# Performance work log

Measured on AMD Instinct MI355X. Metric: run time of the kernel, lower is better.

The kernel has to match this reference:

```python
import jax, jax.numpy as jnp
import numpy as np

NA = 40000   # author nodes
NP = 40000   # paper nodes
E = 800000   # edges per relation
HID = 64
HOP = 5
SEM = 128


def setup_inputs() -> dict:
    key = jax.random.key(0)
    ks = jax.random.split(key, 32)
    f32 = jnp.float32
    rn = lambda k, s, sc=0.1: jax.random.normal(k, s, f32) * sc
    inp = {}
    inp["x_author"] = jax.random.normal(ks[0], (NA, 334), f32)
    inp["x_paper"] = jax.random.normal(ks[1], (NP, 512), f32)
    inp["W1_a"] = rn(ks[2], (334, HID), 0.05)
    inp["b1_a"] = jnp.zeros((HID,), f32)
    inp["W1_p"] = rn(ks[3], (512, HID), 0.05)
    inp["b1_p"] = jnp.zeros((HID,), f32)
    inp["a1_ap"] = rn(ks[4], (HOP, HID))
    inp["a2_ap"] = rn(ks[5], (HOP, HID))
    inp["a1_aa"] = rn(ks[6], (HOP, HID))
    inp["a2_aa"] = rn(ks[7], (HOP, HID))
    inp["a1_pa"] = rn(ks[8], (HOP, HID))
    inp["a2_pa"] = rn(ks[9], (HOP, HID))
    inp["a1_pp"] = rn(ks[10], (HOP, HID))
    inp["a2_pp"] = rn(ks[11], (HOP, HID))
    inp["semW_a"] = rn(ks[12], (HOP, HID, SEM))
    inp["semb_a"] = jnp.zeros((HOP, SEM), f32)
    inp["semq_a"] = rn(ks[13], (HOP, SEM))
    inp["semW_p"] = rn(ks[14], (HOP, HID, SEM))
    inp["semb_p"] = jnp.zeros((HOP, SEM), f32)
    inp["semq_p"] = rn(ks[15], (HOP, SEM))
    inp["W2"] = rn(ks[16], (HID, 4))
    inp["b2"] = jnp.zeros((4,), f32)
    inp["ei_ap"] = jax.random.randint(ks[17], (2, E), 0, NA)  # row0=src(author) row1=tgt(paper)
    inp["ei_aa"] = jax.random.randint(ks[18], (2, E), 0, NA)
    inp["ei_pa"] = jax.random.randint(ks[19], (2, E), 0, NP)
    inp["ei_pp"] = jax.random.randint(ks[20], (2, E), 0, NP)
    return inp


def _leaky(v):
    return jnp.where(v > 0.0, v, 0.2 * v)


def _edge_agg(x, h, s, t, a1, a2, n):
    # x: [Ns,D] source features (fixed), h: [Nt,D] current target state
    x1 = x @ a1                                   # [Ns]
    h1 = h @ a2                                   # [Nt]
    w2 = jnp.exp(_leaky(x1 + x @ a2))             # [Ns] self-loop score
    w1 = jnp.exp(_leaky(x1[s] + h1[t]))           # [E]  edge score
    div = jax.ops.segment_sum(w1, s, num_segments=n) + w2
    num = jax.ops.segment_sum(w1[:, None] * h[t], s, num_segments=n) + w2[:, None] * x
    return num / div[:, None]


def _sem(z, W, b, q):
    # z: [N,M,D]; HAN-style semantic attention over M relations
    sc = jnp.tanh(jnp.einsum('nmd,dk->nmk', z, W) + b) @ q   # [N,M]
    beta = jax.nn.softmax(jnp.mean(sc, axis=0))               # [M]
    return jnp.einsum('m,nmd->nd', beta, z)


def reference(x_author, x_paper, W1_a, b1_a, W1_p, b1_p,
              a1_ap, a2_ap, a1_aa, a2_aa, a1_pa, a2_pa, a1_pp, a2_pp,
              semW_a, semb_a, semq_a, semW_p, semb_p, semq_p,
              W2, b2, ei_ap, ei_aa, ei_pa, ei_pp):
    # eval mode: dropout is identity
    xA = jax.nn.relu(x_author @ W1_a + b1_a)
    xP = jax.nn.relu(x_paper @ W1_p + b1_p)
    hA, hP = xA, xP
    nA, nP = xA.shape[0], xP.shape[0]
    for i in range(HOP):
        eA = jnp.stack([
            _edge_agg(xA, hP, ei_ap[0], ei_ap[1], a1_ap[i], a2_ap[i], nA),
            _edge_agg(xA, hA, ei_aa[0], ei_aa[1], a1_aa[i], a2_aa[i], nA)], axis=1)
        eP = jnp.stack([
            _edge_agg(xP, hA, ei_pa[0], ei_pa[1], a1_pa[i], a2_pa[i], nP),
            _edge_agg(xP, hP, ei_pp[0], ei_pp[1], a1_pp[i], a2_pp[i], nP)], axis=1)
        hA = jax.nn.elu(_sem(eA, semW_a[i], semb_a[i], semq_a[i]))
        hP = jax.nn.elu(_sem(eP, semW_p[i], semb_p[i], semq_p[i]))
    return hA @ W2 + b2   # target_node_type = 'author'
```

## Files before the change

kernel.cpp:

```cpp
#include <hip/hip_runtime.h>
#include <hip/hip_fp16.h>

#define NN 40000
#define DD 64
#define EE 800000
#define NHOP 5
#define NSEM 128
#define NBK 625
#define BINCH 8192

__device__ __forceinline__ float leaky02(float v) { return v > 0.f ? v : 0.2f * v; }
__device__ __forceinline__ float tanh_fast(float x) {
  return 1.f - 2.f / (__expf(2.f * x) + 1.f);
}
__device__ __forceinline__ float wred(float x) {
  #pragma unroll
  for (int m = 1; m < 64; m <<= 1) x += __shfl_xor(x, m);
  return x;
}

__global__ void zero_i32(int* __restrict__ p, int n) {
  int i = blockIdx.x * blockDim.x + threadIdx.x;
  if (i < n) p[i] = 0;
}

#define PBM 64
#define PBK 32
__global__ __launch_bounds__(256) void proj_gemm_relu2(
    const float* __restrict__ Xa, const float* __restrict__ Wa,
    const float* __restrict__ ba, float* __restrict__ oa, __half* __restrict__ oa16,
    const float* __restrict__ Xp, const float* __restrict__ Wp,
    const float* __restrict__ bp, float* __restrict__ op, __half* __restrict__ op16)
{
  int side = blockIdx.y;
  const float* X = side ? Xp : Xa;
  const float* W = side ? Wp : Wa;
  const float* bias = side ? bp : ba;
  float* out = side ? op : oa;
  __half* out16 = side ? op16 : oa16;
  int K = side ? 512 : 334;

  __shared__ float As[PBM][PBK + 1];
  __shared__ float Bs[PBK][DD];
  int tid = threadIdx.x;
  int tx = tid & 15;
  int ty = tid >> 4;
  int row0 = blockIdx.x * PBM;
  float acc[4][4] = {{0.f}};
  int nk = (K + PBK - 1) / PBK;
  for (int kt = 0; kt < nk; ++kt) {
    int k0 = kt * PBK;
    #pragma unroll
    for (int j = 0; j < 8; ++j) {
      int idx = tid + j * 256;
      int r = idx >> 5, c = idx & 31;
      int gk = k0 + c;
      As[r][c] = (gk < K) ? X[(size_t)(row0 + r) * K + gk] : 0.f;
    }
    #pragma unroll
    for (int j = 0; j < 2; ++j) {
      int idx = tid + j * 256;
      int r = idx >> 4, c4 = idx & 15;
      int gk = k0 + r;
      float4 v = (gk < K) ? ((const float4*)(W + (size_t)gk * DD))[c4]
                          : make_float4(0.f, 0.f, 0.f, 0.f);
      ((float4*)&Bs[r][0])[c4] = v;
    }
    __syncthreads();
    #pragma unroll 8
    for (int kk = 0; kk < PBK; ++kk) {
      float a0 = As[ty * 4 + 0][kk];
      float a1 = As[ty * 4 + 1][kk];
      float a2 = As[ty * 4 + 2][kk];
      float a3 = As[ty * 4 + 3][kk];
      float4 bv = ((float4*)&Bs[kk][0])[tx];
      acc[0][0] = fmaf(a0, bv.x, acc[0][0]);
      acc[0][1] = fmaf(a0, bv.y, acc[0][1]);
      acc[0][2] = fmaf(a0, bv.z, acc[0][2]);
      acc[0][3] = fmaf(a0, bv.w, acc[0][3]);
      acc[1][0] = fmaf(a1, bv.x, acc[1][0]);
      acc[1][1] = fmaf(a1, bv.y, acc[1][1]);
      acc[1][2] = fmaf(a1, bv.z, acc[1][2]);
      acc[1][3] = fmaf(a1, bv.w, acc[1][3]);
      acc[2][0] = fmaf(a2, bv.x, acc[2][0]);
      acc[2][1] = fmaf(a2, bv.y, acc[2][1]);
      acc[2][2] = fmaf(a2, bv.z, acc[2][2]);
      acc[2][3] = fmaf(a2, bv.w, acc[2][3]);
      acc[3][0] = fmaf(a3, bv.x, acc[3][0]);
      acc[3][1] = fmaf(a3, bv.y, acc[3][1]);
      acc[3][2] = fmaf(a3, bv.z, acc[3][2]);
      acc[3][3] = fmaf(a3, bv.w, acc[3][3]);
    }
    __syncthreads();
  }
  float4 bb = ((const float4*)bias)[tx];
  #pragma unroll
  for (int i = 0; i < 4; ++i) {
    int gr = row0 + ty * 4 + i;
    float4 v;
    v.x = fmaxf(acc[i][0] + bb.x, 0.f);
    v.y = fmaxf(acc[i][1] + bb.y, 0.f);
    v.z = fmaxf(acc[i][2] + bb.z, 0.f);
    v.w = fmaxf(acc[i][3] + bb.w, 0.f);
    ((float4*)(out + (size_t)gr * DD))[tx] = v;
    __half2 p0 = __floats2half2_rn(v.x, v.y);
    __half2 p1 = __floats2half2_rn(v.z, v.w);
    ((__half2*)(out16 + (size_t)gr * DD))[tx * 2 + 0] = p0;
    ((__half2*)(out16 + (size_t)gr * DD))[tx * 2 + 1] = p1;
  }
}

__global__ __launch_bounds__(256) void binCount_kernel(
    const int* __restrict__ e0, const int* __restrict__ e1,
    const int* __restrict__ e2, const int* __restrict__ e3,
    int* __restrict__ bcnt, int e)
{
  int rel = blockIdx.y;
  const int* S = rel == 0 ? e0 : rel == 1 ? e1 : rel == 2 ? e2 : e3;
  __shared__ int cnt[NBK];
  int tid = threadIdx.x;
  for (int b = tid; b < NBK; b += 256) cnt[b] = 0;
  __syncthreads();
  int e0i = blockIdx.x * BINCH;
  int ne = min(BINCH, e - e0i);
  for (int i = tid; i < ne; i += 256) atomicAdd(&cnt[S[e0i + i] >> 6], 1);
  __syncthreads();
  for (int b = tid; b < NBK; b += 256)
    if (cnt[b]) atomicAdd(&bcnt[rel * NBK + b], cnt[b]);
}

__global__ __launch_bounds__(1024) void bucketScan_kernel(
    const int* __restrict__ bcnt, int* __restrict__ bbase, int* __restrict__ bcur,
    int* __restrict__ rp0, int* __restrict__ rp1, int* __restrict__ rp2,
    int* __restrict__ rp3, int e)
{
  int rel = blockIdx.x;
  __shared__ int sh[1024];
  int t = threadIdx.x;
  int v = (t < NBK) ? bcnt[rel * NBK + t] : 0;
  sh[t] = v;
  __syncthreads();
  for (int off = 1; off < 1024; off <<= 1) {
    int y = (t >= off) ? sh[t - off] : 0;
    __syncthreads();
    sh[t] += y;
    __syncthreads();
  }
  if (t < NBK) {
    int base = sh[t] - v;
    bbase[rel * (NBK + 1) + t] = base;
    bcur[rel * NBK + t] = base;
  }
  if (t == 0) {
    bbase[rel * (NBK + 1) + NBK] = e;
    (rel == 0 ? rp0 : rel == 1 ? rp1 : rel == 2 ? rp2 : rp3)[NN] = e;
  }
}

__global__ __launch_bounds__(256) void binA_kernel(
    const int* __restrict__ e0, const int* __restrict__ e1,
    const int* __restrict__ e2, const int* __restrict__ e3,
    int* __restrict__ bcur, unsigned* __restrict__ pairbuf, int e)
{
  int rel = blockIdx.y;
  const int* S = rel == 0 ? e0 : rel == 1 ? e1 : rel == 2 ? e2 : e3;
  const int* T = S + e;
  unsigned* pb = pairbuf + (size_t)rel * e;
  __shared__ int cnt[NBK], base[NBK], cnt2[NBK];
  int tid = threadIdx.x;
  for (int b = tid; b < NBK; b += 256) { cnt[b] = 0; cnt2[b] = 0; }
  __syncthreads();
  int e0i = blockIdx.x * BINCH;
  int ne = min(BINCH, e - e0i);
  for (int i = tid; i < ne; i += 256) atomicAdd(&cnt[S[e0i + i] >> 6], 1);
  __syncthreads();
  for (int b = tid; b < NBK; b += 256)
    base[b] = cnt[b] ? atomicAdd(&bcur[rel * NBK + b], cnt[b]) : 0;
  __syncthreads();
  for (int i = tid; i < ne; i += 256) {
    int s = S[e0i + i];
    int t = T[e0i + i];
    int b = s >> 6;
    int off = atomicAdd(&cnt2[b], 1);
    pb[base[b] + off] = ((unsigned)(s & 63) << 16) | (unsigned)t;
  }
}

__global__ __launch_bounds__(256) void binB_kernel(
    const unsigned* __restrict__ pairbuf, const int* __restrict__ bbase,
    int* __restrict__ rp0, int* __restrict__ rp1, int* __restrict__ rp2,
    int* __restrict__ rp3,
    unsigned short* __restrict__ ts0, unsigned short* __restrict__ ts1,
    unsigned short* __restrict__ ts2, unsigned short* __restrict__ ts3, int e)
{
  int rel = blockIdx.y;
  int* rowptr = rel == 0 ? rp0 : rel == 1 ? rp1 : rel == 2 ? rp2 : rp3;
  unsigned short* ts = rel == 0 ? ts0 : rel == 1 ? ts1 : rel == 2 ? ts2 : ts3;
  const unsigned* pb = pairbuf + (size_t)rel * e;
  int b = blockIdx.x;
  int bstart = bbase[rel * (NBK + 1) + b];
  int bend   = bbase[rel * (NBK + 1) + b + 1];
  __shared__ int ncnt[64], cur[64];
  int tid = threadIdx.x;
  if (tid < 64) ncnt[tid] = 0;
  __syncthreads();
  for (int i = bstart + tid; i < bend; i += 256)
    atomicAdd(&ncnt[(pb[i] >> 16) & 63], 1);
  __syncthreads();
  if (tid < 64) {
    int v = ncnt[tid];
    int x = v;
    #pragma unroll
    for (int off = 1; off < 64; off <<= 1) {
      int y = __shfl_up(x, off);
      if (tid >= off) x += y;
    }
    int nb = bstart + x - v;
    rowptr[b * 64 + tid] = nb;
    cur[tid] = nb;
  }
  __syncthreads();
  for (int i = bstart + tid; i < bend; i += 256) {
    unsigned u = pb[i];
    int pos = atomicAdd(&cur[(u >> 16) & 63], 1);
    ts[pos] = (unsigned short)(u & 0xffffu);
  }
}

__global__ __launch_bounds__(256) void precompute_xw(
    const float* __restrict__ xA, const float* __restrict__ xP,
    const float* __restrict__ a1_ap, const float* __restrict__ a2_ap,
    const float* __restrict__ a1_aa, const float* __restrict__ a2_aa,
    const float* __restrict__ a1_pa, const float* __restrict__ a2_pa,
    const float* __restrict__ a1_pp, const float* __restrict__ a2_pp,
    float* __restrict__ x1all, float* __restrict__ w2all,
    float* __restrict__ h1_ap, float* __restrict__ h1_aa,
    float* __restrict__ h1_pa, float* __restrict__ h1_pp)
{
  int side = blockIdx.y;
  __shared__ float L[21 * DD];
  int tid = threadIdx.x;
  {
    const float* s0 = side ? a1_pa : a1_ap;
    const float* s1 = side ? a2_pa : a2_ap;
    const float* s2 = side ? a1_pp : a1_aa;
    const float* s3 = side ? a2_pp : a2_aa;
    const float* ex = side ? a2_ap : a2_pa;
    for (int i = tid; i < 21 * DD; i += 256) {
      int k = i >> 6, d = i & 63;
      const float* src = (k < 5) ? s0 : (k < 10) ? s1 : (k < 15) ? s2 : (k < 20) ? s3 : ex;
      int hop = (k < 20) ? (k % 5) : 0;
      L[i] = src[hop * DD + d];
    }
  }
  __syncthreads();
  int j = blockIdx.x * 256 + tid;
  if (j >= NN) return;
  const float4* x4 = (const float4*)((side ? xP : xA) + (size_t)j * DD);
  float acc[21];
  #pragma unroll
  for (int k = 0; k < 21; ++k) acc[k] = 0.f;
  #pragma unroll
  for (int d0 = 0; d0 < 16; ++d0) {
    float4 v = x4[d0];
    #pragma unroll
    for (int c = 0; c < 4; ++c) {
      int d = d0 * 4 + c;
      float xv = (&v.x)[c];
      #pragma unroll
      for (int k = 0; k < 21; ++k) acc[k] = fmaf(xv, L[k * DD + d], acc[k]);
    }
  }
  int relA = side ? 2 : 0;
  #pragma unroll
  for (int i = 0; i < NHOP; ++i) {
    x1all[((size_t)(relA + 0) * NHOP + i) * NN + j] = acc[0 * 5 + i];
    w2all[((size_t)(relA + 0) * NHOP + i) * NN + j] =
        __expf(leaky02(acc[0 * 5 + i] + acc[1 * 5 + i]));
    x1all[((size_t)(relA + 1) * NHOP + i) * NN + j] = acc[2 * 5 + i];
    w2all[((size_t)(relA + 1) * NHOP + i) * NN + j] =
        __expf(leaky02(acc[2 * 5 + i] + acc[3 * 5 + i]));
  }
  if (side) { h1_pp[j] = acc[15]; h1_ap[j] = acc[20]; }
  else      { h1_aa[j] = acc[15]; h1_pa[j] = acc[20]; }
}

struct AggRel {
  const float* x; const __half2* h2; const float* x1; const float* w2; const float* h1;
  const int* rowptr; const unsigned short* tsorted; float* out;
};

__global__ __launch_bounds__(256) void agg4_kernel(AggRel r0, AggRel r1, AggRel r2,
                                                   AggRel r3, int n)
{
  int bid = blockIdx.x;
  int g = (bid >> 2) & 1;
  int u = (bid >> 3) * 4 + (bid & 3);
  int half = n >> 2;
  int relsel = u >= half;
  int nodeblk = relsel ? (u - half) : u;
  AggRel R;
  if (g == 0) R = relsel ? r2 : r1;
  else        R = relsel ? r3 : r0;

  int wid = nodeblk * 4 + (threadIdx.x >> 6);
  int lane = threadIdx.x & 63;
  int pair = lane >> 5;
  int c2 = lane & 31;

  int beg = R.rowptr[wid], end = R.rowptr[wid + 1];
  float x1i = R.x1[wid];
  float2 a0v = make_float2(0.f, 0.f), a1v = make_float2(0.f, 0.f);
  float2 a2v = make_float2(0.f, 0.f), a3v = make_float2(0.f, 0.f);
  float2 a4v = make_float2(0.f, 0.f), a5v = make_float2(0.f, 0.f);
  float2 a6v = make_float2(0.f, 0.f), a7v = make_float2(0.f, 0.f);
  float wsumL = 0.f;
  for (int c = beg; c < end; c += 64) {
    int idx = c + lane;
    int t = 0;
    float wv = 0.f;
    if (idx < end) {
      t = R.tsorted[idx];
      wv = __expf(leaky02(x1i + R.h1[t]));
    }
    wsumL += wv;
    int ne = min(64, end - c);
    for (int j = 0; j < ne; j += 16) {
      int s0 = j + pair,      s1 = j + 2 + pair,  s2 = j + 4 + pair,  s3 = j + 6 + pair;
      int s4 = j + 8 + pair,  s5 = j + 10 + pair, s6 = j + 12 + pair, s7 = j + 14 + pair;
      int t0 = __shfl(t, s0), t1 = __shfl(t, s1), t2 = __shfl(t, s2), t3 = __shfl(t, s3);
      int t4 = __shfl(t, s4), t5 = __shfl(t, s5), t6 = __shfl(t, s6), t7 = __shfl(t, s7);
      float w0 = __shfl(wv, s0), w1 = __shfl(wv, s1), w2_ = __shfl(wv, s2), w3 = __shfl(wv, s3);
      float w4 = __shfl(wv, s4), w5 = __shfl(wv, s5), w6 = __shfl(wv, s6), w7 = __shfl(wv, s7);
      float2 f0 = __half22float2(R.h2[((unsigned)t0 << 5) + c2]);
      float2 f1 = __half22float2(R.h2[((unsigned)t1 << 5) + c2]);
      float2 f2 = __half22float2(R.h2[((unsigned)t2 << 5) + c2]);
      float2 f3 = __half22float2(R.h2[((unsigned)t3 << 5) + c2]);
      float2 f4 = __half22float2(R.h2[((unsigned)t4 << 5) + c2]);
      float2 f5 = __half22float2(R.h2[((unsigned)t5 << 5) + c2]);
      float2 f6 = __half22float2(R.h2[((unsigned)t6 << 5) + c2]);
      float2 f7 = __half22float2(R.h2[((unsigned)t7 << 5) + c2]);
      a0v.x = fmaf(w0, f0.x, a0v.x);  a0v.y = fmaf(w0, f0.y, a0v.y);
      a1v.x = fmaf(w1, f1.x, a1v.x);  a1v.y = fmaf(w1, f1.y, a1v.y);
      a2v.x = fmaf(w2_, f2.x, a2v.x); a2v.y = fmaf(w2_, f2.y, a2v.y);
      a3v.x = fmaf(w3, f3.x, a3v.x);  a3v.y = fmaf(w3, f3.y, a3v.y);
      a4v.x = fmaf(w4, f4.x, a4v.x);  a4v.y = fmaf(w4, f4.y, a4v.y);
      a5v.x = fmaf(w5, f5.x, a5v.x);  a5v.y = fmaf(w5, f5.y, a5v.y);
      a6v.x = fmaf(w6, f6.x, a6v.x);  a6v.y = fmaf(w6, f6.y, a6v.y);
      a7v.x = fmaf(w7, f7.x, a7v.x);  a7v.y = fmaf(w7, f7.y, a7v.y);
    }
  }
  float wsum = wred(wsumL);
  float2 acc;
  acc.x = ((a0v.x + a1v.x) + (a2v.x + a3v.x)) + ((a4v.x + a5v.x) + (a6v.x + a7v.x));
  acc.y = ((a0v.y + a1v.y) + (a2v.y + a3v.y)) + ((a4v.y + a5v.y) + (a6v.y + a7v.y));
  acc.x += __shfl_xor(acc.x, 32);
  acc.y += __shfl_xor(acc.y, 32);
  if (pair == 0) {
    float w2v = R.w2[wid];
    float inv = 1.f / (wsum + w2v);
    float2 xv = ((const float2*)(R.x + (size_t)wid * DD))[c2];
    float2 o;
    o.x = fmaf(w2v, xv.x, acc.x) * inv;
    o.y = fmaf(w2v, xv.y, acc.y) * inv;
    ((float2*)(R.out + (size_t)wid * DD))[c2] = o;
  }
}

__global__ __launch_bounds__(256) void sem_kernel(
    const float* __restrict__ eA0, const float* __restrict__ eA1,
    const float* __restrict__ eP0, const float* __restrict__ eP1,
    const float* __restrict__ Wa, const float* __restrict__ ba, const float* __restrict__ qa,
    const float* __restrict__ Wp, const float* __restrict__ bp, const float* __restrict__ qp,
    float* __restrict__ psums)
{
  int side = blockIdx.y;
  const float* e0 = side ? eP0 : eA0;
  const float* e1 = side ? eP1 : eA1;
  const float* W = side ? Wp : Wa;
  const float* b = side ? bp : ba;
  const float* q = side ? qp : qa;

  __shared__ float Ws[DD * NSEM];
  __shared__ float zt[2][DD][12];
  __shared__ float red0[256], red1[256];
  int tid = threadIdx.x;
  {
    const float4* W4 = (const float4*)W;
    float4* Ws4 = (float4*)Ws;
    #pragma unroll
    for (int j = 0; j < 8; ++j) Ws4[tid + j * 256] = W4[tid + j * 256];
  }
  int slot = tid >> 7;
  int k = tid & 127;
  float bk = b[k], qk = q[k];
  int base = blockIdx.x * 64;
  float sum0 = 0.f, sum1 = 0.f;
  for (int it = 0; it < 8; ++it) {
    #pragma unroll
    for (int j = 0; j < 4; ++j) {
      int idx = tid + j * 256;
      int d = idx & 63, m = (idx >> 6) & 1, nn = idx >> 7;
      zt[m][d][nn] = (m ? e1 : e0)[(size_t)(base + it * 8 + nn) * DD + d];
    }
    __syncthreads();
    float a0[4], a1[4];
    #pragma unroll
    for (int nn = 0; nn < 4; ++nn) { a0[nn] = bk; a1[nn] = bk; }
    #pragma unroll 8
    for (int d = 0; d < DD; ++d) {
      float w = Ws[d * NSEM + k];
      float4 za = *(const float4*)&zt[0][d][slot * 4];
      float4 zb = *(const float4*)&zt[1][d][slot * 4];
      a0[0] = fmaf(za.x, w, a0[0]);
      a0[1] = fmaf(za.y, w, a0[1]);
      a0[2] = fmaf(za.z, w, a0[2]);
      a0[3] = fmaf(za.w, w, a0[3]);
      a1[0] = fmaf(zb.x, w, a1[0]);
      a1[1] = fmaf(zb.y, w, a1[1]);
      a1[2] = fmaf(zb.z, w, a1[2]);
      a1[3] = fmaf(zb.w, w, a1[3]);
    }
    #pragma unroll
    for (int nn = 0; nn < 4; ++nn) {
      sum0 += tanh_fast(a0[nn]) * qk;
      sum1 += tanh_fast(a1[nn]) * qk;
    }
    __syncthreads();
  }
  red0[tid] = sum0;
  red1[tid] = sum1;
  __syncthreads();
  for (int off = 128; off; off >>= 1) {
    if (tid < off) { red0[tid] += red0[tid + off]; red1[tid] += red1[tid + off]; }
    __syncthreads();
  }
  if (tid == 0) {
    int idx = (side * gridDim.x + blockIdx.x) * 2;
    psums[idx + 0] = red0[0];
    psums[idx + 1] = red1[0];
  }
}

__global__ __launch_bounds__(256) void beta_kernel(const float* __restrict__ psums,
    float* __restrict__ beta, int nblk, float invn)
{
  __shared__ float s[4][256];
  int t = threadIdx.x;
  float a0 = 0.f, a1 = 0.f, p0 = 0.f, p1 = 0.f;
  for (int i = t; i < nblk; i += 256) {
    a0 += psums[i * 2];
    a1 += psums[i * 2 + 1];
    p0 += psums[(nblk + i) * 2];
    p1 += psums[(nblk + i) * 2 + 1];
  }
  s[0][t] = a0; s[1][t] = a1; s[2][t] = p0; s[3][t] = p1;
  __syncthreads();
  for (int off = 128; off; off >>= 1) {
    if (t < off) {
      s[0][t] += s[0][t + off]; s[1][t] += s[1][t + off];
      s[2][t] += s[2][t + off]; s[3][t] += s[3][t + off];
    }
    __syncthreads();
  }
  if (t == 0) {
    float m0 = s[0][0] * invn, m1 = s[1][0] * invn;
    float mx = fmaxf(m0, m1);
    float x0 = __expf(m0 - mx), x1 = __expf(m1 - mx);
    float inv = 1.f / (x0 + x1);
    beta[0] = x0 * inv; beta[1] = x1 * inv;
    m0 = s[2][0] * invn; m1 = s[3][0] * invn;
    mx = fmaxf(m0, m1);
    x0 = __expf(m0 - mx); x1 = __expf(m1 - mx);
    inv = 1.f / (x0 + x1);
    beta[2] = x0 * inv; beta[3] = x1 * inv;
  }
}

__global__ void combine2_kernel(const float4* __restrict__ eA0, const float4* __restrict__ eA1,
    const float4* __restrict__ eP0, const float4* __restrict__ eP1,
    const float* __restrict__ beta, float4* __restrict__ hA, float4* __restrict__ hP,
    __half2* __restrict__ hA16, __half2* __restrict__ hP16,
    const float* __restrict__ a2_ap_n, const float* __restrict__ a2_aa_n,
    const float* __restrict__ a2_pa_n, const float* __restrict__ a2_pp_n,
    float* __restrict__ h1_ap, float* __restrict__ h1_aa,
    float* __restrict__ h1_pa, float* __restrict__ h1_pp,
    int has_next, int nvec)
{
  int side = blockIdx.y;
  int i = blockIdx.x * 256 + threadIdx.x;
  if (i >= nvec) return;
  float b0 = beta[side * 2], b1 = beta[side * 2 + 1];
  float4 v0 = (side ? eP0 : eA0)[i];
  float4 v1 = (side ? eP1 : eA1)[i];
  float4 r;
  float t;
  t = b0 * v0.x + b1 * v1.x; r.x = t > 0.f ? t : (__expf(t) - 1.f);
  t = b0 * v0.y + b1 * v1.y; r.y = t > 0.f ? t : (__expf(t) - 1.f);
  t = b0 * v0.z + b1 * v1.z; r.z = t > 0.f ? t : (__expf(t) - 1.f);
  t = b0 * v0.w + b1 * v1.w; r.w = t > 0.f ? t : (__expf(t) - 1.f);
  (side ? hP : hA)[i] = r;
  (side ? hP16 : hA16)[i * 2 + 0] = __floats2half2_rn(r.x, r.y);
  (side ? hP16 : hA16)[i * 2 + 1] = __floats2half2_rn(r.z, r.w);
  if (has_next) {
    int col4 = i & 15;
    const float* ax = side ? a2_ap_n : a2_aa_n;
    const float* ay = side ? a2_pp_n : a2_pa_n;
    float4 a4 = ((const float4*)ax)[col4];
    float4 c4 = ((const float4*)ay)[col4];
    float rx = r.x * a4.x + r.y * a4.y + r.z * a4.z + r.w * a4.w;
    float ry = r.x * c4.x + r.y * c4.y + r.z * c4.z + r.w * c4.w;
    #pragma unroll
    for (int m = 1; m < 16; m <<= 1) {
      rx += __shfl_xor(rx, m);
      ry += __shfl_xor(ry, m);
    }
    if ((threadIdx.x & 15) == 0) {
      int row = i >> 4;
      if (side) { h1_ap[row] = rx; h1_pp[row] = ry; }
      else      { h1_aa[row] = rx; h1_pa[row] = ry; }
    }
  }
}

__global__ void final_kernel(const float* __restrict__ hA, const float* __restrict__ W2,
    const float* __restrict__ b2, float* __restrict__ out, int n)
{
  int j = blockIdx.x * blockDim.x + threadIdx.x;
  if (j >= n) return;
  float acc0 = b2[0], acc1 = b2[1], acc2 = b2[2], acc3 = b2[3];
  const float4* hrow = (const float4*)(hA + (size_t)j * DD);
  #pragma unroll
  for (int d4 = 0; d4 < 16; ++d4) {
    float4 v = hrow[d4];
    #pragma unroll
    for (int c = 0; c < 4; ++c) {
      int d = d4 * 4 + c;
      float vv = (&v.x)[c];
      acc0 = fmaf(vv, W2[d * 4 + 0], acc0);
      acc1 = fmaf(vv, W2[d * 4 + 1], acc1);
      acc2 = fmaf(vv, W2[d * 4 + 2], acc2);
      acc3 = fmaf(vv, W2[d * 4 + 3], acc3);
    }
  }
  ((float4*)out)[j] = make_float4(acc0, acc1, acc2, acc3);
}

extern "C" void kernel_launch(void* const* d_in, const int* in_sizes, int n_in,
                              void* d_out, int out_size, void* d_ws, size_t ws_size,
                              hipStream_t stream)
{
  const float* x_author = (const float*)d_in[0];
  const float* x_paper  = (const float*)d_in[1];
  const float* W1_a = (const float*)d_in[2];
  const float* b1_a = (const float*)d_in[3];
  const float* W1_p = (const float*)d_in[4];
  const float* b1_p = (const float*)d_in[5];
  const float* a1_ap = (const float*)d_in[6];
  const float* a2_ap = (const float*)d_in[7];
  const float* a1_aa = (const float*)d_in[8];
  const float* a2_aa = (const float*)d_in[9];
  const float* a1_pa = (const float*)d_in[10];
  const float* a2_pa = (const float*)d_in[11];
  const float* a1_pp = (const float*)d_in[12];
  const float* a2_pp = (const float*)d_in[13];
  const float* semW_a = (const float*)d_in[14];
  const float* semb_a = (const float*)d_in[15];
  const float* semq_a = (const float*)d_in[16];
  const float* semW_p = (const float*)d_in[17];
  const float* semb_p = (const float*)d_in[18];
  const float* semq_p = (const float*)d_in[19];
  const float* W2 = (const float*)d_in[20];
  const float* b2 = (const float*)d_in[21];
  const int* ei[4] = {(const int*)d_in[22], (const int*)d_in[23],
                      (const int*)d_in[24], (const int*)d_in[25]};

  char* w = (char*)d_ws;
  auto alloc = [&](size_t bytes) -> void* {
    void* p = (void*)w;
    w += (bytes + 255) & ~(size_t)255;
    return p;
  };
  const size_t matB = (size_t)NN * DD * sizeof(float);
  float* xA  = (float*)alloc(matB);
  float* xP  = (float*)alloc(matB);
  float* hA  = (float*)alloc(matB);
  float* hP  = (float*)alloc(matB);
  float* eA0 = (float*)alloc(matB);
  float* eA1 = (float*)alloc(matB);
  float* eP0 = (float*)alloc(matB);
  float* eP1 = (float*)alloc(matB);
  __half* xA16 = (__half*)alloc(matB / 2);
  __half* xP16 = (__half*)alloc(matB / 2);
  __half* hA16 = xA16;
  __half* hP16 = xP16;
  unsigned* pairbuf = (unsigned*)eA0;
  int* rowptr[4]; unsigned short* tsorted[4];
  for (int r = 0; r < 4; ++r) {
    rowptr[r]  = (int*)alloc((NN + 1) * sizeof(int));
    tsorted[r] = (unsigned short*)alloc((size_t)EE * sizeof(unsigned short));
  }
  int* bcnt  = (int*)alloc((size_t)4 * NBK * sizeof(int));
  int* bbase = (int*)alloc((size_t)4 * (NBK + 1) * sizeof(int));
  int* bcur  = (int*)alloc((size_t)4 * NBK * sizeof(int));
  float* x1all = (float*)alloc((size_t)4 * NHOP * NN * sizeof(float));
  float* w2all = (float*)alloc((size_t)4 * NHOP * NN * sizeof(float));
  float* h1b[4];
  for (int r = 0; r < 4; ++r) h1b[r] = (float*)alloc(NN * sizeof(float));
  float* psums = (float*)alloc((size_t)2 * NBK * 2 * sizeof(float));
  float* betab = (float*)alloc(64);

  proj_gemm_relu2<<<dim3(NN / PBM, 2), 256, 0, stream>>>(
      x_author, W1_a, b1_a, xA, xA16,
      x_paper,  W1_p, b1_p, xP, xP16);

  const int NEB = (EE + BINCH - 1) / BINCH;
  zero_i32<<<(4 * NBK + 255) / 256, 256, 0, stream>>>(bcnt, 4 * NBK);
  binCount_kernel<<<dim3(NEB, 4), 256, 0, stream>>>(ei[0], ei[1], ei[2], ei[3], bcnt, EE);
  bucketScan_kernel<<<4, 1024, 0, stream>>>(bcnt, bbase, bcur,
      rowptr[0], rowptr[1], rowptr[2], rowptr[3], EE);
  binA_kernel<<<dim3(NEB, 4), 256, 0, stream>>>(
      ei[0], ei[1], ei[2], ei[3], bcur, pairbuf, EE);
  binB_kernel<<<dim3(NBK, 4), 256, 0, stream>>>(pairbuf, bbase,
      rowptr[0], rowptr[1], rowptr[2], rowptr[3],
      tsorted[0], tsorted[1], tsorted[2], tsorted[3], EE);

  precompute_xw<<<dim3((NN + 255) / 256, 2), 256, 0, stream>>>(
      xA, xP, a1_ap, a2_ap, a1_aa, a2_aa, a1_pa, a2_pa, a1_pp, a2_pp,
      x1all, w2all, h1b[0], h1b[1], h1b[2], h1b[3]);

  const int CVEC = NN * DD / 4;
  for (int i = 0; i < NHOP; ++i) {
    #define X1(r) (x1all + ((size_t)(r) * NHOP + i) * NN)
    #define W2P(r) (w2all + ((size_t)(r) * NHOP + i) * NN)
    AggRel r0 = {xA, (const __half2*)hP16, X1(0), W2P(0), h1b[0], rowptr[0], tsorted[0], eA0};
    AggRel r1 = {xA, (const __half2*)hA16, X1(1), W2P(1), h1b[1], rowptr[1], tsorted[1], eA1};
    AggRel r2 = {xP, (const __half2*)hA16, X1(2), W2P(2), h1b[2], rowptr[2], tsorted[2], eP0};
    AggRel r3 = {xP, (const __half2*)hP16, X1(3), W2P(3), h1b[3], rowptr[3], tsorted[3], eP1};
    agg4_kernel<<<NN, 256, 0, stream>>>(r0, r1, r2, r3, NN);

    sem_kernel<<<dim3(NN / 64, 2), 256, 0, stream>>>(
        eA0, eA1, eP0, eP1,
        semW_a + (size_t)i * DD * NSEM, semb_a + i * NSEM, semq_a + i * NSEM,
        semW_p + (size_t)i * DD * NSEM, semb_p + i * NSEM, semq_p + i * NSEM,
        psums);
    beta_kernel<<<1, 256, 0, stream>>>(psums, betab, NN / 64, 1.f / NN);

    int inext = (i + 1 < NHOP) ? (i + 1) : i;
    combine2_kernel<<<dim3((CVEC + 255) / 256, 2), 256, 0, stream>>>(
        (const float4*)eA0, (const float4*)eA1, (const float4*)eP0, (const float4*)eP1,
        betab, (float4*)hA, (float4*)hP, (__half2*)hA16, (__half2*)hP16,
        a2_ap + inext * DD, a2_aa + inext * DD, a2_pa + inext * DD, a2_pp + inext * DD,
        h1b[0], h1b[1], h1b[2], h1b[3], (i + 1 < NHOP) ? 1 : 0, CVEC);
  }

  final_kernel<<<(NN + 255) / 256, 256, 0, stream>>>(hA, W2, b2, (float*)d_out, NN);
}
```

Baseline: 942.8 us.

## Fold beta softmax into sem kernel via last-block counter; shrink projection GEMM tiles

Removes the separate beta_kernel launch each hop. The last sem_kernel block to finish, found through an atomic counter, reduces the partial sums and computes the softmax weights, then resets the counter. Separately, the projection GEMM now uses 32-row tiles with 128-thread blocks, doubling the block count. The fused path adds threadfence and atomic overhead and relies on the counter being zeroed at setup.

```diff
diff --git a/kernel.cpp b/kernel.cpp
--- a/kernel.cpp
+++ b/kernel.cpp
@@ -24,9 +24,8 @@
   if (i < n) p[i] = 0;
 }
 
-#define PBM 64
 #define PBK 32
-__global__ __launch_bounds__(256) void proj_gemm_relu2(
+__global__ __launch_bounds__(128) void proj_gemm_relu2(
     const float* __restrict__ Xa, const float* __restrict__ Wa,
     const float* __restrict__ ba, float* __restrict__ oa, __half* __restrict__ oa16,
     const float* __restrict__ Xp, const float* __restrict__ Wp,
@@ -40,26 +39,26 @@
   __half* out16 = side ? op16 : oa16;
   int K = side ? 512 : 334;
 
-  __shared__ float As[PBM][PBK + 1];
+  __shared__ float As[32][PBK + 1];
   __shared__ float Bs[PBK][DD];
   int tid = threadIdx.x;
   int tx = tid & 15;
   int ty = tid >> 4;
-  int row0 = blockIdx.x * PBM;
+  int row0 = blockIdx.x * 32;
   float acc[4][4] = {{0.f}};
   int nk = (K + PBK - 1) / PBK;
   for (int kt = 0; kt < nk; ++kt) {
     int k0 = kt * PBK;
     #pragma unroll
     for (int j = 0; j < 8; ++j) {
-      int idx = tid + j * 256;
+      int idx = tid + j * 128;
       int r = idx >> 5, c = idx & 31;
       int gk = k0 + c;
       As[r][c] = (gk < K) ? X[(size_t)(row0 + r) * K + gk] : 0.f;
     }
     #pragma unroll
-    for (int j = 0; j < 2; ++j) {
-      int idx = tid + j * 256;
+    for (int j = 0; j < 4; ++j) {
+      int idx = tid + j * 128;
       int r = idx >> 4, c4 = idx & 15;
       int gk = k0 + r;
       float4 v = (gk < K) ? ((const float4*)(W + (size_t)gk * DD))[c4]
@@ -372,7 +371,7 @@
     const float* __restrict__ eP0, const float* __restrict__ eP1,
     const float* __restrict__ Wa, const float* __restrict__ ba, const float* __restrict__ qa,
     const float* __restrict__ Wp, const float* __restrict__ bp, const float* __restrict__ qp,
-    float* __restrict__ psums)
+    float* __restrict__ psums, float* __restrict__ beta, int* __restrict__ ctr)
 {
   int side = blockIdx.y;
   const float* e0 = side ? eP0 : eA0;
@@ -440,40 +439,45 @@
     psums[idx + 0] = red0[0];
     psums[idx + 1] = red1[0];
   }
-}
-
-__global__ __launch_bounds__(256) void beta_kernel(const float* __restrict__ psums,
-    float* __restrict__ beta, int nblk, float invn)
-{
-  __shared__ float s[4][256];
-  int t = threadIdx.x;
+  __threadfence();
+  __shared__ int lastFlag;
+  if (tid == 0)
+    lastFlag = (atomicAdd(ctr, 1) == (int)(2 * gridDim.x) - 1);
+  __syncthreads();
+  if (!lastFlag) return;
+  __threadfence();
+  int nblk = gridDim.x;
   float a0 = 0.f, a1 = 0.f, p0 = 0.f, p1 = 0.f;
-  for (int i = t; i < nblk; i += 256) {
+  for (int i = tid; i < nblk; i += 256) {
     a0 += psums[i * 2];
     a1 += psums[i * 2 + 1];
     p0 += psums[(nblk + i) * 2];
     p1 += psums[(nblk + i) * 2 + 1];
   }
-  s[0][t] = a0; s[1][t] = a1; s[2][t] = p0; s[3][t] = p1;
+  float* red2 = &zt[0][0][0];
+  float* red3 = red2 + 256;
+  red0[tid] = a0; red1[tid] = a1; red2[tid] = p0; red3[tid] = p1;
   __syncthreads();
   for (int off = 128; off; off >>= 1) {
-    if (t < off) {
-      s[0][t] += s[0][t + off]; s[1][t] += s[1][t + off];
-      s[2][t] += s[2][t + off]; s[3][t] += s[3][t + off];
-    }
-    __syncthreads();
-  }
-  if (t == 0) {
-    float m0 = s[0][0] * invn, m1 = s[1][0] * invn;
+    if (tid < off) {
+      red0[tid] += red0[tid + off]; red1[tid] += red1[tid + off];
+      red2[tid] += red2[tid + off]; red3[tid] += red3[tid + off];
+    }
+    __syncthreads();
+  }
+  if (tid == 0) {
+    float invn = 1.f / NN;
+    float m0 = red0[0] * invn, m1 = red1[0] * invn;
     float mx = fmaxf(m0, m1);
     float x0 = __expf(m0 - mx), x1 = __expf(m1 - mx);
     float inv = 1.f / (x0 + x1);
     beta[0] = x0 * inv; beta[1] = x1 * inv;
-    m0 = s[2][0] * invn; m1 = s[3][0] * invn;
+    m0 = red2[0] * invn; m1 = red3[0] * invn;
     mx = fmaxf(m0, m1);
     x0 = __expf(m0 - mx); x1 = __expf(m1 - mx);
     inv = 1.f / (x0 + x1);
     beta[2] = x0 * inv; beta[3] = x1 * inv;
+    *ctr = 0;
   }
 }
 
@@ -600,7 +604,8 @@
     rowptr[r]  = (int*)alloc((NN + 1) * sizeof(int));
     tsorted[r] = (unsigned short*)alloc((size_t)EE * sizeof(unsigned short));
   }
-  int* bcnt  = (int*)alloc((size_t)4 * NBK * sizeof(int));
+  int* bcnt  = (int*)alloc(((size_t)4 * NBK + 64) * sizeof(int));
+  int* semctr = bcnt + 4 * NBK;
   int* bbase = (int*)alloc((size_t)4 * (NBK + 1) * sizeof(int));
   int* bcur  = (int*)alloc((size_t)4 * NBK * sizeof(int));
   float* x1all = (float*)alloc((size_t)4 * NHOP * NN * sizeof(float));
@@ -610,12 +615,12 @@
   float* psums = (float*)alloc((size_t)2 * NBK * 2 * sizeof(float));
   float* betab = (float*)alloc(64);
 
-  proj_gemm_relu2<<<dim3(NN / PBM, 2), 256, 0, stream>>>(
+  proj_gemm_relu2<<<dim3(NN / 32, 2), 128, 0, stream>>>(
       x_author, W1_a, b1_a, xA, xA16,
       x_paper,  W1_p, b1_p, xP, xP16);
 
   const int NEB = (EE + BINCH - 1) / BINCH;
-  zero_i32<<<(4 * NBK + 255) / 256, 256, 0, stream>>>(bcnt, 4 * NBK);
+  zero_i32<<<(4 * NBK + 64 + 255) / 256, 256, 0, stream>>>(bcnt, 4 * NBK + 64);
   binCount_kernel<<<dim3(NEB, 4), 256, 0, stream>>>(ei[0], ei[1], ei[2], ei[3], bcnt, EE);
   bucketScan_kernel<<<4, 1024, 0, stream>>>(bcnt, bbase, bcur,
       rowptr[0], rowptr[1], rowptr[2], rowptr[3], EE);
@@ -643,8 +648,7 @@
         eA0, eA1, eP0, eP1,
         semW_a + (size_t)i * DD * NSEM, semb_a + i * NSEM, semq_a + i * NSEM,
         semW_p + (size_t)i * DD * NSEM, semb_p + i * NSEM, semq_p + i * NSEM,
-        psums);
-    beta_kernel<<<1, 256, 0, stream>>>(psums, betab, NN / 64, 1.f / NN);
+        psums, betab, semctr);
 
     int inext = (i + 1 < NHOP) ? (i + 1) : i;
     combine2_kernel<<<dim3((CVEC + 255) / 256, 2), 256, 0, stream>>>(
```

New measurement: 1.372 ms. 1.46x slower.
